# Kernel tuning notes

Measured on AMD Instinct MI355X. Metric: run time of the kernel, lower is better.

The kernel has to match this reference:

```python
import jax, jax.numpy as jnp
import numpy as np

EPS = 1e-10

def setup_inputs() -> dict:
    key = jax.random.key(0)
    kq, kk, kv = jax.random.split(key, 3)
    B, S, D = 8, 4096, 64
    q = jax.random.normal(kq, (B, S, D), dtype=jnp.float32)
    k = jax.random.normal(kk, (B, S, D), dtype=jnp.float32)
    v = jax.random.normal(kv, (B, S, D), dtype=jnp.float32)
    attention_mask = jnp.zeros((B, S, S), dtype=bool)
    return {"q": q, "k": k, "v": v, "attention_mask": attention_mask}

def reference(q, k, v, attention_mask):
    # L2-normalize q and k along feature dim (norm + eps in denominator, per torch code)
    q = q / (jnp.linalg.norm(q, axis=-1, keepdims=True) + EPS)
    k = k / (jnp.linalg.norm(k, axis=-1, keepdims=True) + EPS)
    # [B, S, S] cosine similarity scores
    scores = jnp.einsum('bqd,bkd->bqk', q, k)
    scores = jnp.where(attention_mask, -jnp.inf, scores)
    soft_attention = jax.nn.softmax(scores, axis=-1)
    # dropout_rate = 0.0 -> identity
    output = jnp.einsum('bqk,bkd->bqd', soft_attention, v)
    return (output, soft_attention)
```

## Files before the change

kernel.cpp:

```cpp
#include <hip/hip_runtime.h>
#include <math.h>

#define BB 8
#define SS 4096
#define DD 64
#define NT (SS / 64)

typedef float  f32x4 __attribute__((ext_vector_type(4)));
typedef short  s16x4 __attribute__((ext_vector_type(4)));
typedef short  s16x8 __attribute__((ext_vector_type(8)));
typedef unsigned char u8x16 __attribute__((ext_vector_type(16)));

__device__ __forceinline__ short f2bf(float f) {
  unsigned u = __builtin_bit_cast(unsigned, f);
  u += 0x7FFFu + ((u >> 16) & 1u);
  return (short)(u >> 16);
}

__global__ __launch_bounds__(256) void k_norm(const float* __restrict__ q,
                                              const float* __restrict__ k,
                                              short* __restrict__ qn,
                                              short* __restrict__ kn) {
  const long BS = (long)BB * SS;
  long row = (long)blockIdx.x * 4 + (threadIdx.x >> 6);
  int lane = threadIdx.x & 63;
  const float* src;
  short* dst;
  if (row < BS) { src = q + row * DD; dst = qn + row * DD; }
  else          { src = k + (row - BS) * DD; dst = kn + (row - BS) * DD; }
  float x = src[lane];
  float ss = x * x;
#pragma unroll
  for (int m = 32; m >= 1; m >>= 1) ss += __shfl_xor(ss, m);
  float inv = 1.0f / (sqrtf(ss) + 1e-10f);
  dst[lane] = f2bf(x * inv);
}

__global__ __launch_bounds__(256) void k_vtrans(const float* __restrict__ v,
                                                short* __restrict__ vt) {
  __shared__ short tile[64][65];
  int b = blockIdx.y;
  int s0 = blockIdx.x * 64;
  const float* V = v + ((long)b * SS + s0) * DD;
  int t = threadIdx.x;
#pragma unroll
  for (int i = 0; i < 16; i++) {
    int flat = t + 256 * i;
    int sl = flat >> 6, d = flat & 63;
    tile[sl][d] = f2bf(V[flat]);
  }
  __syncthreads();
  short* VT = vt + (long)b * DD * SS + s0;
#pragma unroll
  for (int i = 0; i < 16; i++) {
    int flat = t + 256 * i;
    int d = flat >> 6, sl = flat & 63;
    VT[(long)d * SS + sl] = tile[sl][d];
  }
}

__global__ __launch_bounds__(256) void k_maskbits(const unsigned char* __restrict__ m,
                                                  unsigned short* __restrict__ bits) {
  long gid = (long)blockIdx.x * 256 + threadIdx.x;
  u8x16 v = __builtin_nontemporal_load((const u8x16*)(m + gid * 16));
  unsigned r = 0;
#pragma unroll
  for (int i = 0; i < 16; i++) r |= (v[i] ? 1u : 0u) << i;
  __builtin_nontemporal_store((unsigned short)r, bits + gid);
}

__global__ __launch_bounds__(256) void k_rowsum(const short* __restrict__ qn,
                                                const short* __restrict__ kn,
                                                const unsigned short* __restrict__ bits,
                                                float* __restrict__ inv_sum) {
  __shared__ __align__(16) short Kt[2][4096];
  int b = blockIdx.x & 7;
  int q0 = (blockIdx.x >> 3) << 6;
  int wid = threadIdx.x >> 6, lane = threadIdx.x & 63;
  int l15 = lane & 15, g = lane >> 4;
  int qr = q0 + (wid << 4);

  const short* Qr = qn + ((long)(b * SS) + qr + l15) * DD;
  s16x8 qf0 = *(const s16x8*)(Qr + 8 * g);
  s16x8 qf1 = *(const s16x8*)(Qr + 32 + 8 * g);

  const short* Kb = kn + (long)b * SS * DD;
  const unsigned long long* B64 =
      (const unsigned long long*)bits + ((long)(b * SS) + qr + l15) * (SS / 64);

  int sr = lane >> 3, sc = lane & 7;
  int r0 = (wid << 4) + sr, r1 = r0 + 8;
  const short* Ksrc0 = Kb + (long)r0 * DD + sc * 8;
  const short* Ksrc1 = Kb + (long)r1 * DD + sc * 8;
  int kd0 = r0 * DD + ((sc ^ sr) << 3);
  int kd1 = r1 * DD + ((sc ^ sr) << 3);

  s16x8 kst0 = *(const s16x8*)Ksrc0;
  s16x8 kst1 = *(const s16x8*)Ksrc1;
  *(s16x8*)&Kt[0][kd0] = kst0;
  *(s16x8*)&Kt[0][kd1] = kst1;
  __syncthreads();

  float acc = 0.f;
  int cur = 0;
  int swk = (l15 & 7);
  for (int t = 0; t < NT; ++t) {
    if (t + 1 < NT) {
      long koff = (long)(t + 1) * 64 * DD;
      kst0 = *(const s16x8*)(Ksrc0 + koff);
      kst1 = *(const s16x8*)(Ksrc1 + koff);
    }
    unsigned long long w64 = B64[t];
    const short* Kc = &Kt[cur][0];
#pragma unroll
    for (int tt = 0; tt < 4; ++tt) {
      const short* krow = Kc + ((tt << 4) + l15) * DD;
      s16x8 a0 = *(const s16x8*)(krow + ((g ^ swk) << 3));
      s16x8 a1 = *(const s16x8*)(krow + (((4 + g) ^ swk) << 3));
      f32x4 c = {0.f, 0.f, 0.f, 0.f};
      c = __builtin_amdgcn_mfma_f32_16x16x32_bf16(a0, qf0, c, 0, 0, 0);
      c = __builtin_amdgcn_mfma_f32_16x16x32_bf16(a1, qf1, c, 0, 0, 0);
#pragma unroll
      for (int r = 0; r < 4; ++r) {
        unsigned bit = (unsigned)(w64 >> ((tt << 4) + (g << 2) + r)) & 1u;
        acc += bit ? 0.f : __expf(c[r]);
      }
    }
    if (t + 1 < NT) {
      short* Kd = &Kt[cur ^ 1][0];
      *(s16x8*)(Kd + kd0) = kst0;
      *(s16x8*)(Kd + kd1) = kst1;
    }
    __syncthreads();
    cur ^= 1;
  }
  acc += __shfl_xor(acc, 16);
  acc += __shfl_xor(acc, 32);
  if (lane < 16) inv_sum[(long)b * SS + qr + l15] = 1.0f / acc;
}

__global__ __launch_bounds__(256) void k_attn(const short* __restrict__ qn,
                                              const short* __restrict__ kn,
                                              const short* __restrict__ vt,
                                              const unsigned short* __restrict__ bits,
                                              const float* __restrict__ inv_sum,
                                              float* __restrict__ O,
                                              float* __restrict__ P) {
  __shared__ __align__(16) short Kt[2][4096];
  __shared__ __align__(16) short Vt[2][4096];
  int b = blockIdx.x & 7;
  int q0 = (blockIdx.x >> 3) << 6;
  int wid = threadIdx.x >> 6, lane = threadIdx.x & 63;
  int l15 = lane & 15, g = lane >> 4;
  int qr = q0 + (wid << 4);

  const short* Qr = qn + ((long)(b * SS) + qr + l15) * DD;
  s16x8 qf0 = *(const s16x8*)(Qr + 8 * g);
  s16x8 qf1 = *(const s16x8*)(Qr + 32 + 8 * g);

  const short* Kb = kn + (long)b * SS * DD;
  const short* Vb = vt + (long)b * DD * SS;
  const unsigned long long* B64 =
      (const unsigned long long*)bits + ((long)(b * SS) + qr + l15) * (SS / 64);
  float inv = inv_sum[(long)b * SS + qr + l15];
  float linv = __logf(inv);
  float* Prow = P + ((long)(b * SS) + qr + l15) * SS;

  int sr = lane >> 3, sc = lane & 7;
  int r0 = (wid << 4) + sr, r1 = r0 + 8;
  const short* Ksrc0 = Kb + (long)r0 * DD + sc * 8;
  const short* Ksrc1 = Kb + (long)r1 * DD + sc * 8;
  const short* Vsrc0 = Vb + (long)r0 * SS + sc * 8;
  const short* Vsrc1 = Vb + (long)r1 * SS + sc * 8;
  int sd0 = r0 * DD + ((sc ^ sr) << 3);
  int sd1 = r1 * DD + ((sc ^ sr) << 3);

  s16x8 kst0 = *(const s16x8*)Ksrc0;
  s16x8 kst1 = *(const s16x8*)Ksrc1;
  s16x8 vst0 = *(const s16x8*)Vsrc0;
  s16x8 vst1 = *(const s16x8*)Vsrc1;
  *(s16x8*)&Kt[0][sd0] = kst0;
  *(s16x8*)&Kt[0][sd1] = kst1;
  *(s16x8*)&Vt[0][sd0] = vst0;
  *(s16x8*)&Vt[0][sd1] = vst1;
  __syncthreads();

  f32x4 o0 = {0, 0, 0, 0}, o1 = {0, 0, 0, 0}, o2 = {0, 0, 0, 0}, o3 = {0, 0, 0, 0};
  int cur = 0;
  int swk = (l15 & 7);
  for (int t = 0; t < NT; ++t) {
    if (t + 1 < NT) {
      long koff = (long)(t + 1) * 64 * DD;
      kst0 = *(const s16x8*)(Ksrc0 + koff);
      kst1 = *(const s16x8*)(Ksrc1 + koff);
      vst0 = *(const s16x8*)(Vsrc0 + (t + 1) * 64);
      vst1 = *(const s16x8*)(Vsrc1 + (t + 1) * 64);
    }
    unsigned long long w64 = B64[t];
    const short* Kc = &Kt[cur][0];
    const short* Vc = &Vt[cur][0];

    f32x4 p[4];
#pragma unroll
    for (int tt = 0; tt < 4; ++tt) {
      const short* krow = Kc + ((tt << 4) + l15) * DD;
      s16x8 a0 = *(const s16x8*)(krow + ((g ^ swk) << 3));
      s16x8 a1 = *(const s16x8*)(krow + (((4 + g) ^ swk) << 3));
      f32x4 c = {0.f, 0.f, 0.f, 0.f};
      c = __builtin_amdgcn_mfma_f32_16x16x32_bf16(a0, qf0, c, 0, 0, 0);
      c = __builtin_amdgcn_mfma_f32_16x16x32_bf16(a1, qf1, c, 0, 0, 0);
#pragma unroll
      for (int r = 0; r < 4; ++r) {
        unsigned bit = (unsigned)(w64 >> ((tt << 4) + (g << 2) + r)) & 1u;
        p[tt][r] = bit ? 0.f : __expf(c[r] + linv);
      }
      __builtin_nontemporal_store(p[tt],
          (f32x4*)(Prow + (t << 6) + (tt << 4) + (g << 2)));
    }

    s16x8 pa0, pa1;
#pragma unroll
    for (int j = 0; j < 4; ++j) {
      pa0[j] = f2bf(p[0][j]); pa0[4 + j] = f2bf(p[1][j]);
      pa1[j] = f2bf(p[2][j]); pa1[4 + j] = f2bf(p[3][j]);
    }

#pragma unroll
    for (int n = 0; n < 4; ++n) {
      const short* vrow = Vc + ((n << 4) + l15) * DD;
      int g2 = g >> 1, hh = (g & 1) << 2;
      s16x4 lo0 = *(const s16x4*)(vrow + (((g2    ) ^ swk) << 3) + hh);
      s16x4 hi0 = *(const s16x4*)(vrow + (((g2 + 2) ^ swk) << 3) + hh);
      s16x4 lo1 = *(const s16x4*)(vrow + (((g2 + 4) ^ swk) << 3) + hh);
      s16x4 hi1 = *(const s16x4*)(vrow + (((g2 + 6) ^ swk) << 3) + hh);
      s16x8 vf0 = __builtin_shufflevector(lo0, hi0, 0, 1, 2, 3, 4, 5, 6, 7);
      s16x8 vf1 = __builtin_shufflevector(lo1, hi1, 0, 1, 2, 3, 4, 5, 6, 7);
      f32x4* on = (n == 0) ? &o0 : (n == 1) ? &o1 : (n == 2) ? &o2 : &o3;
      *on = __builtin_amdgcn_mfma_f32_16x16x32_bf16(pa0, vf0, *on, 0, 0, 0);
      *on = __builtin_amdgcn_mfma_f32_16x16x32_bf16(pa1, vf1, *on, 0, 0, 0);
    }

    if (t + 1 < NT) {
      short* Kd = &Kt[cur ^ 1][0];
      short* Vd = &Vt[cur ^ 1][0];
      *(s16x8*)(Kd + sd0) = kst0;
      *(s16x8*)(Kd + sd1) = kst1;
      *(s16x8*)(Vd + sd0) = vst0;
      *(s16x8*)(Vd + sd1) = vst1;
    }
    __syncthreads();
    cur ^= 1;
  }

  float* Ob = O + ((long)(b * SS) + qr) * DD;
#pragma unroll
  for (int r = 0; r < 4; ++r) {
    int row = (g << 2) + r;
    Ob[row * DD +  0 + l15] = o0[r];
    Ob[row * DD + 16 + l15] = o1[r];
    Ob[row * DD + 32 + l15] = o2[r];
    Ob[row * DD + 48 + l15] = o3[r];
  }
}

extern "C" void kernel_launch(void* const* d_in, const int* in_sizes, int n_in,
                              void* d_out, int out_size, void* d_ws, size_t ws_size,
                              hipStream_t stream) {
  const float* q = (const float*)d_in[0];
  const float* k = (const float*)d_in[1];
  const float* v = (const float*)d_in[2];
  const unsigned char* mask = (const unsigned char*)d_in[3];

  const long BSD = (long)BB * SS * DD;
  short* qn = (short*)d_ws;
  short* kn = qn + BSD;
  short* vtp = kn + BSD;
  float* inv_sum = (float*)(vtp + BSD);
  unsigned short* bits = (unsigned short*)(inv_sum + (long)BB * SS);

  float* O = (float*)d_out;
  float* P = O + BSD;

  k_norm<<<dim3(2 * BB * SS / 4), dim3(256), 0, stream>>>(q, k, qn, kn);
  k_vtrans<<<dim3(SS / 64, BB), dim3(256), 0, stream>>>(v, vtp);
  k_maskbits<<<dim3((int)((long)BB * SS * SS / 16 / 256)), dim3(256), 0, stream>>>(mask, bits);
  k_rowsum<<<dim3(BB * SS / 64), dim3(256), 0, stream>>>(qn, kn, bits, inv_sum);
  k_attn<<<dim3(BB * SS / 64), dim3(256), 0, stream>>>(qn, kn, vtp, bits, inv_sum, O, P);
}
```

Measured before the change: 252.7 us.

## Fuse preprocessing kernels, use packed bf16 convert, and relax loop barrier

Merges the mask-bit packing, q/k normalization and V transpose kernels into one launch dispatched by block index, saving two kernel launches and the gaps between them. In the attention kernel, the per-element bf16 rounding of probabilities is replaced by the hardware packed convert instruction. The __syncthreads at the end of each loop iteration becomes an explicit LDS wait plus a raw s_barrier. The workspace layout is also reordered. The hardware convert may round slightly differently from the software routine, and the raw barrier depends on global loads not needing a vmcnt wait at that point.

```diff
diff --git a/kernel.cpp b/kernel.cpp
--- a/kernel.cpp
+++ b/kernel.cpp
@@ -6,6 +6,9 @@
 #define DD 64
 #define NT (SS / 64)
 
+#define NMB 32768
+#define NNB 16384
+
 typedef float  f32x4 __attribute__((ext_vector_type(4)));
 typedef short  s16x4 __attribute__((ext_vector_type(4)));
 typedef short  s16x8 __attribute__((ext_vector_type(8)));
@@ -17,32 +20,54 @@
   return (short)(u >> 16);
 }
 
-__global__ __launch_bounds__(256) void k_norm(const float* __restrict__ q,
-                                              const float* __restrict__ k,
-                                              short* __restrict__ qn,
-                                              short* __restrict__ kn) {
-  const long BS = (long)BB * SS;
-  long row = (long)blockIdx.x * 4 + (threadIdx.x >> 6);
-  int lane = threadIdx.x & 63;
-  const float* src;
-  short* dst;
-  if (row < BS) { src = q + row * DD; dst = qn + row * DD; }
-  else          { src = k + (row - BS) * DD; dst = kn + (row - BS) * DD; }
-  float x = src[lane];
-  float ss = x * x;
-#pragma unroll
-  for (int m = 32; m >= 1; m >>= 1) ss += __shfl_xor(ss, m);
-  float inv = 1.0f / (sqrtf(ss) + 1e-10f);
-  dst[lane] = f2bf(x * inv);
-}
-
-__global__ __launch_bounds__(256) void k_vtrans(const float* __restrict__ v,
-                                                short* __restrict__ vt) {
+__device__ __forceinline__ unsigned pk_bf16(float lo, float hi) {
+  unsigned r;
+  asm("v_cvt_pk_bf16_f32 %0, %1, %2" : "=v"(r) : "v"(lo), "v"(hi));
+  return r;
+}
+
+__global__ __launch_bounds__(256) void k_pre(const float* __restrict__ q,
+                                             const float* __restrict__ k,
+                                             const float* __restrict__ v,
+                                             const unsigned char* __restrict__ mask,
+                                             short* __restrict__ qn,
+                                             short* __restrict__ kn,
+                                             short* __restrict__ vt,
+                                             unsigned short* __restrict__ bits) {
   __shared__ short tile[64][65];
-  int b = blockIdx.y;
-  int s0 = blockIdx.x * 64;
+  int blk = blockIdx.x;
+  int t = threadIdx.x;
+
+  if (blk < NMB) {
+    long gid = (long)blk * 256 + t;
+    u8x16 mv = __builtin_nontemporal_load((const u8x16*)(mask + gid * 16));
+    unsigned r = 0;
+#pragma unroll
+    for (int i = 0; i < 16; i++) r |= (mv[i] ? 1u : 0u) << i;
+    __builtin_nontemporal_store((unsigned short)r, bits + gid);
+    return;
+  }
+  blk -= NMB;
+  if (blk < NNB) {
+    const long BS = (long)BB * SS;
+    long row = (long)blk * 4 + (t >> 6);
+    int lane = t & 63;
+    const float* src;
+    short* dst;
+    if (row < BS) { src = q + row * DD; dst = qn + row * DD; }
+    else          { src = k + (row - BS) * DD; dst = kn + (row - BS) * DD; }
+    float x = src[lane];
+    float ss = x * x;
+#pragma unroll
+    for (int m = 32; m >= 1; m >>= 1) ss += __shfl_xor(ss, m);
+    float inv = 1.0f / (sqrtf(ss) + 1e-10f);
+    dst[lane] = f2bf(x * inv);
+    return;
+  }
+  blk -= NNB;
+  int b = blk >> 6;
+  int s0 = (blk & 63) << 6;
   const float* V = v + ((long)b * SS + s0) * DD;
-  int t = threadIdx.x;
 #pragma unroll
   for (int i = 0; i < 16; i++) {
     int flat = t + 256 * i;
@@ -57,16 +82,6 @@
     int d = flat >> 6, sl = flat & 63;
     VT[(long)d * SS + sl] = tile[sl][d];
   }
-}
-
-__global__ __launch_bounds__(256) void k_maskbits(const unsigned char* __restrict__ m,
-                                                  unsigned short* __restrict__ bits) {
-  long gid = (long)blockIdx.x * 256 + threadIdx.x;
-  u8x16 v = __builtin_nontemporal_load((const u8x16*)(m + gid * 16));
-  unsigned r = 0;
-#pragma unroll
-  for (int i = 0; i < 16; i++) r |= (v[i] ? 1u : 0u) << i;
-  __builtin_nontemporal_store((unsigned short)r, bits + gid);
 }
 
 __global__ __launch_bounds__(256) void k_rowsum(const short* __restrict__ qn,
@@ -94,6 +109,7 @@
   const short* Ksrc1 = Kb + (long)r1 * DD + sc * 8;
   int kd0 = r0 * DD + ((sc ^ sr) << 3);
   int kd1 = r1 * DD + ((sc ^ sr) << 3);
+  int swk = l15 & 7;
 
   s16x8 kst0 = *(const s16x8*)Ksrc0;
   s16x8 kst1 = *(const s16x8*)Ksrc1;
@@ -103,7 +119,6 @@
 
   float acc = 0.f;
   int cur = 0;
-  int swk = (l15 & 7);
   for (int t = 0; t < NT; ++t) {
     if (t + 1 < NT) {
       long koff = (long)(t + 1) * 64 * DD;
@@ -174,6 +189,7 @@
   const short* Vsrc1 = Vb + (long)r1 * SS + sc * 8;
   int sd0 = r0 * DD + ((sc ^ sr) << 3);
   int sd1 = r1 * DD + ((sc ^ sr) << 3);
+  int swk = l15 & 7;
 
   s16x8 kst0 = *(const s16x8*)Ksrc0;
   s16x8 kst1 = *(const s16x8*)Ksrc1;
@@ -187,7 +203,6 @@
 
   f32x4 o0 = {0, 0, 0, 0}, o1 = {0, 0, 0, 0}, o2 = {0, 0, 0, 0}, o3 = {0, 0, 0, 0};
   int cur = 0;
-  int swk = (l15 & 7);
   for (int t = 0; t < NT; ++t) {
     if (t + 1 < NT) {
       long koff = (long)(t + 1) * 64 * DD;
@@ -218,12 +233,15 @@
           (f32x4*)(Prow + (t << 6) + (tt << 4) + (g << 2)));
     }
 
-    s16x8 pa0, pa1;
-#pragma unroll
-    for (int j = 0; j < 4; ++j) {
-      pa0[j] = f2bf(p[0][j]); pa0[4 + j] = f2bf(p[1][j]);
-      pa1[j] = f2bf(p[2][j]); pa1[4 + j] = f2bf(p[3][j]);
-    }
+    union { s16x8 v; unsigned u[4]; } pa0, pa1;
+    pa0.u[0] = pk_bf16(p[0][0], p[0][1]);
+    pa0.u[1] = pk_bf16(p[0][2], p[0][3]);
+    pa0.u[2] = pk_bf16(p[1][0], p[1][1]);
+    pa0.u[3] = pk_bf16(p[1][2], p[1][3]);
+    pa1.u[0] = pk_bf16(p[2][0], p[2][1]);
+    pa1.u[1] = pk_bf16(p[2][2], p[2][3]);
+    pa1.u[2] = pk_bf16(p[3][0], p[3][1]);
+    pa1.u[3] = pk_bf16(p[3][2], p[3][3]);
 
 #pragma unroll
     for (int n = 0; n < 4; ++n) {
@@ -236,8 +254,8 @@
       s16x8 vf0 = __builtin_shufflevector(lo0, hi0, 0, 1, 2, 3, 4, 5, 6, 7);
       s16x8 vf1 = __builtin_shufflevector(lo1, hi1, 0, 1, 2, 3, 4, 5, 6, 7);
       f32x4* on = (n == 0) ? &o0 : (n == 1) ? &o1 : (n == 2) ? &o2 : &o3;
-      *on = __builtin_amdgcn_mfma_f32_16x16x32_bf16(pa0, vf0, *on, 0, 0, 0);
-      *on = __builtin_amdgcn_mfma_f32_16x16x32_bf16(pa1, vf1, *on, 0, 0, 0);
+      *on = __builtin_amdgcn_mfma_f32_16x16x32_bf16(pa0.v, vf0, *on, 0, 0, 0);
+      *on = __builtin_amdgcn_mfma_f32_16x16x32_bf16(pa1.v, vf1, *on, 0, 0, 0);
     }
 
     if (t + 1 < NT) {
@@ -248,7 +266,9 @@
       *(s16x8*)(Vd + sd0) = vst0;
       *(s16x8*)(Vd + sd1) = vst1;
     }
-    __syncthreads();
+    asm volatile("s_waitcnt lgkmcnt(0)" ::: "memory");
+    __builtin_amdgcn_sched_barrier(0);
+    __builtin_amdgcn_s_barrier();
     cur ^= 1;
   }
 
@@ -275,15 +295,14 @@
   short* qn = (short*)d_ws;
   short* kn = qn + BSD;
   short* vtp = kn + BSD;
-  float* inv_sum = (float*)(vtp + BSD);
-  unsigned short* bits = (unsigned short*)(inv_sum + (long)BB * SS);
+  unsigned short* bits = (unsigned short*)(vtp + BSD);
+  float* inv_sum = (float*)(bits + (long)BB * SS * 256);
 
   float* O = (float*)d_out;
   float* P = O + BSD;
 
-  k_norm<<<dim3(2 * BB * SS / 4), dim3(256), 0, stream>>>(q, k, qn, kn);
-  k_vtrans<<<dim3(SS / 64, BB), dim3(256), 0, stream>>>(v, vtp);
-  k_maskbits<<<dim3((int)((long)BB * SS * SS / 16 / 256)), dim3(256), 0, stream>>>(mask, bits);
+  k_pre<<<dim3(NMB + NNB + SS / 64 * BB), dim3(256), 0, stream>>>(
+      q, k, v, mask, qn, kn, vtp, bits);
   k_rowsum<<<dim3(BB * SS / 64), dim3(256), 0, stream>>>(qn, kn, bits, inv_sum);
   k_attn<<<dim3(BB * SS / 64), dim3(256), 0, stream>>>(qn, kn, vtp, bits, inv_sum, O, P);
 }
```

Result: slower. 281.7 us (+11.5%).
